# Performance work log

Measured on AMD Instinct MI355X. Metric: run time of the kernel, lower is better.

The kernel has to match this reference:

```python
import jax, jax.numpy as jnp
import numpy as np
import math

HIDDEN = 384
HEADS = 4
HEAD_DIM = HIDDEN // HEADS
B, T = 8, 2048


def _shift_rel(pos_tensor):
    # pos_tensor: [b, h, t, 2t-1] -> [b, h, t, t] (Transformer-XL shift trick)
    b, h, t, n = pos_tensor.shape
    zero_pad = jnp.zeros((b, h, t, 1), dtype=pos_tensor.dtype)
    padded = jnp.concatenate([zero_pad, pos_tensor], axis=-1)  # [b,h,t,n+1]
    padded = padded.reshape(b, h, n + 1, t)
    shifted = padded[:, :, 1:].reshape(b, h, t, n)
    return shifted[:, :, :, : n // 2 + 1]  # [b,h,t,t]


def setup_inputs() -> dict:
    key = jax.random.key(0)
    ks = jax.random.split(key, 12)
    s = 1.0 / math.sqrt(HIDDEN)
    inp = {
        "hidden_states": jax.random.normal(ks[0], (B, T, HIDDEN), jnp.float32),
        "pos_emb": jax.random.normal(ks[1], (1, 2 * T - 1, HIDDEN), jnp.float32),
        "attention_mask": jnp.ones((B, 1, T), jnp.int32),
        "Wq": jax.random.normal(ks[2], (HIDDEN, HIDDEN), jnp.float32) * s,
        "bq": jnp.zeros((HIDDEN,), jnp.float32),
        "Wk": jax.random.normal(ks[3], (HIDDEN, HIDDEN), jnp.float32) * s,
        "bk": jnp.zeros((HIDDEN,), jnp.float32),
        "Wv": jax.random.normal(ks[4], (HIDDEN, HIDDEN), jnp.float32) * s,
        "bv": jnp.zeros((HIDDEN,), jnp.float32),
        "Wo": jax.random.normal(ks[5], (HIDDEN, HIDDEN), jnp.float32) * s,
        "bo": jnp.zeros((HIDDEN,), jnp.float32),
        "Wpos": jax.random.normal(ks[6], (HIDDEN, HIDDEN), jnp.float32) * s,
        "pos_bias_u": jax.random.normal(ks[7], (HEADS, HEAD_DIM), jnp.float32) * s,
        "pos_bias_v": jax.random.normal(ks[8], (HEADS, HEAD_DIM), jnp.float32) * s,
    }
    return inp


def reference(hidden_states, pos_emb, attention_mask, Wq, bq, Wk, bk, Wv, bv,
              Wo, bo, Wpos, pos_bias_u, pos_bias_v):
    bsz, q_len, _ = hidden_states.shape
    # projections (nn.Linear applies x @ W.T + b; weights here stored as [in, out])
    q = (hidden_states @ Wq + bq).reshape(bsz, q_len, HEADS, HEAD_DIM)
    k = (hidden_states @ Wk + bk).reshape(bsz, q_len, HEADS, HEAD_DIM)
    v = (hidden_states @ Wv + bv).reshape(bsz, q_len, HEADS, HEAD_DIM)
    pos = (pos_emb @ Wpos).reshape(pos_emb.shape[0], -1, HEADS, HEAD_DIM)

    q_u = (q + pos_bias_u).transpose(0, 2, 1, 3)  # [b,h,t,d]
    q_v = (q + pos_bias_v).transpose(0, 2, 1, 3)

    # content score: [b,h,t,t]
    matrix_ac = jnp.einsum('bhqd,bkhd->bhqk', q_u, k)
    # position score: [b,h,t,2t-1] then shift
    matrix_bd = jnp.einsum('bhqd,pnhd->bhqn', q_v, pos)
    matrix_bd = _shift_rel(matrix_bd)

    scores = (matrix_ac + matrix_bd) / math.sqrt(HEAD_DIM)

    mask = (attention_mask[:, None] == 0)  # [b,1,1,t]
    min_val = jnp.finfo(scores.dtype).min
    scores = jnp.where(mask, min_val, scores)
    attn = jax.nn.softmax(scores, axis=-1)
    attn = jnp.where(mask, 0.0, attn)

    out = jnp.einsum('bhqk,bkhd->bqhd', attn, v).reshape(bsz, q_len, HIDDEN)
    return out @ Wo + bo
```

## Files before the change

kernel.cpp:

```cpp
#include <hip/hip_runtime.h>
#include <hip/hip_bf16.h>

#define TSEQ 2048
#define HID 384
#define NHEAD 4
#define HD 96
#define NBATCH 8

using bf16 = __bf16;
typedef bf16 bf16x8 __attribute__((ext_vector_type(8)));
typedef bf16 bf16x4 __attribute__((ext_vector_type(4)));
typedef float f32x4 __attribute__((ext_vector_type(4)));
typedef unsigned long long u64;

static __device__ __forceinline__ f32x4 mfma16(bf16x8 a, bf16x8 b, f32x4 c) {
    return __builtin_amdgcn_mfma_f32_16x16x32_bf16(a, b, c, 0, 0, 0);
}

#define LDS_HANDOFF()                                   \
    __builtin_amdgcn_sched_barrier(0x7F);               \
    asm volatile("s_waitcnt lgkmcnt(0)");               \
    __builtin_amdgcn_sched_barrier(0x7F)

#define GL2LDS(g, l) __builtin_amdgcn_global_load_lds(                        \
    (const __attribute__((address_space(1))) unsigned int*)(const void*)(g),  \
    (__attribute__((address_space(3))) unsigned int*)(void*)(l), 16, 0, 0)

__global__ void k_conv8(const float* __restrict__ src, bf16* __restrict__ dst, int n8) {
    int t = blockIdx.x * 256 + threadIdx.x;
    if (t >= n8) return;
    const float4* s4 = reinterpret_cast<const float4*>(src);
    float4 a = s4[2 * t], b = s4[2 * t + 1];
    bf16x8 o;
    o[0] = (bf16)a.x; o[1] = (bf16)a.y; o[2] = (bf16)a.z; o[3] = (bf16)a.w;
    o[4] = (bf16)b.x; o[5] = (bf16)b.y; o[6] = (bf16)b.z; o[7] = (bf16)b.w;
    *reinterpret_cast<bf16x8*>(dst + 8 * t) = o;
}

__global__ void k_convT5(const float* __restrict__ W0, const float* __restrict__ W1,
                         const float* __restrict__ W2, const float* __restrict__ W3,
                         const float* __restrict__ W4,
                         bf16* __restrict__ T0, bf16* __restrict__ T1,
                         bf16* __restrict__ T2, bf16* __restrict__ T3,
                         bf16* __restrict__ T4) {
    int t = blockIdx.x * 256 + threadIdx.x;
    int which = blockIdx.y;
    const float* W = (which == 0) ? W0 : (which == 1) ? W1 : (which == 2) ? W2
                     : (which == 3) ? W3 : W4;
    bf16* T = (which == 0) ? T0 : (which == 1) ? T1 : (which == 2) ? T2
              : (which == 3) ? T3 : T4;
    int n = t / HID, k = t % HID;
    T[t] = (bf16)W[(size_t)k * HID + n];
}

__launch_bounds__(256, 2)
__global__ void k_proj(const bf16* __restrict__ X, const bf16* __restrict__ P,
                       const bf16* __restrict__ wqT, const bf16* __restrict__ wkT,
                       const bf16* __restrict__ wvT, const bf16* __restrict__ wpT,
                       const float* __restrict__ bq, const float* __restrict__ bk,
                       const float* __restrict__ bv,
                       const float* __restrict__ pbu, const float* __restrict__ pbv,
                       bf16* __restrict__ qu, bf16* __restrict__ qv,
                       bf16* __restrict__ kws, bf16* __restrict__ vt,
                       bf16* __restrict__ pp) {
    __shared__ bf16 wt_lds[96][392];
    const float SC = 0.10206207262f;
    int mat = blockIdx.z;
    int m0 = blockIdx.x * 64;
    if (mat == 3 && m0 >= 4095) return;
    int n0 = blockIdx.y * 96;
    const bf16* A  = (mat == 3) ? P : X;
    const bf16* WT = (mat == 0) ? wqT : (mat == 1) ? wkT : (mat == 2) ? wvT : wpT;
    int tid = threadIdx.x;
    #pragma unroll
    for (int s = 0; s < 18; ++s) {
        int cc = tid + 256 * s;
        int r = cc / 48, ch = cc % 48;
        *reinterpret_cast<int4*>(&wt_lds[r][ch * 8]) =
            *reinterpret_cast<const int4*>(WT + (size_t)(n0 + r) * HID + ch * 8);
    }
    __syncthreads();
    int lane = tid & 63, w = tid >> 6;
    int c = lane & 15, g = lane >> 4;
    int arow = m0 + 16 * w + c;
    if (mat == 3 && arow > 4095) arow = 4095;
    const bf16* Abase = A + (size_t)arow * HID + 8 * g;
    f32x4 acc[6] = {};
    for (int ks = 0; ks < 12; ++ks) {
        bf16x8 a = *reinterpret_cast<const bf16x8*>(Abase + 32 * ks);
        #pragma unroll
        for (int jt = 0; jt < 6; ++jt) {
            bf16x8 b = *reinterpret_cast<const bf16x8*>(&wt_lds[16 * jt + c][32 * ks + 8 * g]);
            acc[jt] = mfma16(a, b, acc[jt]);
        }
    }
    int h = blockIdx.y;
    int rbase = m0 + 16 * w + 4 * g;
    if (mat == 0) {
        #pragma unroll
        for (int jt = 0; jt < 6; ++jt) {
            int n = n0 + 16 * jt + c;
            int d = 16 * jt + c;
            float bb = bq[n], bu = pbu[n], bvv = pbv[n];
            #pragma unroll
            for (int j = 0; j < 4; ++j) {
                int m = rbase + j;
                int b_ = m >> 11, t = m & 2047;
                size_t o = (((size_t)(b_ * NHEAD + h)) * TSEQ + t) * HD + d;
                float q = acc[jt][j] + bb;
                qu[o] = (bf16)((q + bu) * SC);
                qv[o] = (bf16)((q + bvv) * SC);
            }
        }
    } else if (mat == 1) {
        #pragma unroll
        for (int jt = 0; jt < 6; ++jt) {
            int n = n0 + 16 * jt + c;
            int d = 16 * jt + c;
            float bb = bk[n];
            #pragma unroll
            for (int j = 0; j < 4; ++j) {
                int m = rbase + j;
                int b_ = m >> 11, t = m & 2047;
                size_t o = (((size_t)(b_ * NHEAD + h)) * TSEQ + t) * HD + d;
                kws[o] = (bf16)(acc[jt][j] + bb);
            }
        }
    } else if (mat == 2) {
        #pragma unroll
        for (int jt = 0; jt < 6; ++jt) {
            int d = 16 * jt + c;
            float bb = bv[n0 + 16 * jt + c];
            int m = rbase;
            int b_ = m >> 11, t0 = m & 2047;
            size_t o = (((size_t)(b_ * NHEAD + h)) * HD + d) * TSEQ + t0;
            bf16x4 pk;
            #pragma unroll
            for (int j = 0; j < 4; ++j) pk[j] = (bf16)(acc[jt][j] + bb);
            *reinterpret_cast<bf16x4*>(vt + o) = pk;
        }
    } else {
        #pragma unroll
        for (int jt = 0; jt < 6; ++jt) {
            int d = 16 * jt + c;
            #pragma unroll
            for (int j = 0; j < 4; ++j) {
                int m = rbase + j;
                if (m < 4095) {
                    size_t o = ((size_t)h * 4096 + m) * HD + d;
                    pp[o] = (bf16)acc[jt][j];
                }
            }
        }
    }
}

__launch_bounds__(256, 2)
__global__ void k_attn(const bf16* __restrict__ qu, const bf16* __restrict__ qv,
                       const bf16* __restrict__ kws, const bf16* __restrict__ vt,
                       const bf16* __restrict__ pp, const int* __restrict__ mask,
                       bf16* __restrict__ out) {
    __shared__ bf16 k_lds[128][104];
    __shared__ bf16 vt_lds[96][128];
    __shared__ bf16 wp_lds[4][16][168];

    int bid = blockIdx.x;
    int x = bid & 7, j5 = bid >> 3;
    int h = x & 3;
    int b_ = (x >> 2) * 4 + (j5 >> 5);
    int qb = j5 & 31;
    int bh = b_ * NHEAD + h;
    int q0 = qb * 64;

    int tid = threadIdx.x, lane = tid & 63, w = tid >> 6;
    int c = lane & 15, g = lane >> 4;
    const float L2E = 1.44269504089f;
    const int NB = 2032 - q0 - 16 * w;

    bf16* k_flat = &k_lds[0][0];
    bf16* vt_flat = &vt_lds[0][0];
    int cc0 = tid, cc1 = tid + 256, cc2 = tid + 512, cc3 = tid + 768;
    int cc4 = tid + 1024, cc5 = tid + 1280, cc6 = tid + 1536;
    int kr0 = cc0 / 13, kc0 = cc0 % 13;  int kO0 = kr0 * HD + (kc0 == 12 ? 0 : kc0 * 8);
    int kr1 = cc1 / 13, kc1 = cc1 % 13;  int kO1 = kr1 * HD + (kc1 == 12 ? 0 : kc1 * 8);
    int kr2 = cc2 / 13, kc2 = cc2 % 13;  int kO2 = kr2 * HD + (kc2 == 12 ? 0 : kc2 * 8);
    int kr3 = cc3 / 13, kc3 = cc3 % 13;  int kO3 = kr3 * HD + (kc3 == 12 ? 0 : kc3 * 8);
    int kr4 = cc4 / 13, kc4 = cc4 % 13;  int kO4 = kr4 * HD + (kc4 == 12 ? 0 : kc4 * 8);
    int kr5 = cc5 / 13, kc5 = cc5 % 13;  int kO5 = kr5 * HD + (kc5 == 12 ? 0 : kc5 * 8);
    int kr6 = cc6 / 13, kc6 = cc6 % 13;  int kO6 = kr6 * HD + (kc6 == 12 ? 0 : kc6 * 8);
    bf16* kL0 = k_flat + (size_t)(64 * w + 0)    * 8;
    bf16* kL1 = k_flat + (size_t)(64 * w + 256)  * 8;
    bf16* kL2 = k_flat + (size_t)(64 * w + 512)  * 8;
    bf16* kL3 = k_flat + (size_t)(64 * w + 768)  * 8;
    bf16* kL4 = k_flat + (size_t)(64 * w + 1024) * 8;
    bf16* kL5 = k_flat + (size_t)(64 * w + 1280) * 8;
    bf16* kL6 = k_flat + (size_t)(64 * w + 1536) * 8;
    bool kAct6 = (w < 2);
    int vr0 = cc0 >> 4, vc0 = cc0 & 15;  int vO0 = vr0 * TSEQ + (vc0 ^ (vr0 & 7)) * 8;
    int vr1 = cc1 >> 4, vc1 = cc1 & 15;  int vO1 = vr1 * TSEQ + (vc1 ^ (vr1 & 7)) * 8;
    int vr2 = cc2 >> 4, vc2 = cc2 & 15;  int vO2 = vr2 * TSEQ + (vc2 ^ (vr2 & 7)) * 8;
    int vr3 = cc3 >> 4, vc3 = cc3 & 15;  int vO3 = vr3 * TSEQ + (vc3 ^ (vr3 & 7)) * 8;
    int vr4 = cc4 >> 4, vc4 = cc4 & 15;  int vO4 = vr4 * TSEQ + (vc4 ^ (vr4 & 7)) * 8;
    int vr5 = cc5 >> 4, vc5 = cc5 & 15;  int vO5 = vr5 * TSEQ + (vc5 ^ (vr5 & 7)) * 8;
    bf16* vL0 = vt_flat + (size_t)(64 * w + 0)    * 8;
    bf16* vL1 = vt_flat + (size_t)(64 * w + 256)  * 8;
    bf16* vL2 = vt_flat + (size_t)(64 * w + 512)  * 8;
    bf16* vL3 = vt_flat + (size_t)(64 * w + 768)  * 8;
    bf16* vL4 = vt_flat + (size_t)(64 * w + 1024) * 8;
    bf16* vL5 = vt_flat + (size_t)(64 * w + 1280) * 8;

    const bf16* kbP = kws + (size_t)bh * TSEQ * HD;
    const bf16* vbP = vt + (size_t)bh * HD * TSEQ;
    const bf16* pbP = pp + (size_t)h * 4096 * HD;
    const int*  mbP = mask + b_ * TSEQ;

    bf16x8 qu_f[3], qv_f[3];
    {
        size_t rowbase = ((size_t)bh * TSEQ + q0 + 16 * w + c) * HD + 8 * g;
        #pragma unroll
        for (int ds = 0; ds < 3; ++ds) {
            qu_f[ds] = *reinterpret_cast<const bf16x8*>(qu + rowbase + 32 * ds);
            qv_f[ds] = *reinterpret_cast<const bf16x8*>(qv + rowbase + 32 * ds);
        }
    }

    f32x4 acc_o[6] = {};
    float mrow = -3.0e38f, lrow = 0.f;
    f32x4 wc;
    int   mk0, mk1;

    bf16* wp_row = &wp_lds[w][c][0];
    const int hc = (15 - c) >> 2;
    const int sh = ((15 - c) & 3) * 16;

    auto winpair = [&](int wb, int ta, int tb) {
        f32x4 wa = {}, wbv = {};
        const bf16* pa = pbP + (size_t)(wb + 16 * ta + c) * HD + 8 * g;
        const bf16* pb = pbP + (size_t)(wb + 16 * tb + c) * HD + 8 * g;
        __builtin_amdgcn_s_setprio(1);
        #pragma unroll
        for (int ds = 0; ds < 3; ++ds) {
            wa  = mfma16(*reinterpret_cast<const bf16x8*>(pa + 32 * ds), qv_f[ds], wa);
            wbv = mfma16(*reinterpret_cast<const bf16x8*>(pb + 32 * ds), qv_f[ds], wbv);
        }
        __builtin_amdgcn_s_setprio(0);
        bf16x4 qa, qb;
        #pragma unroll
        for (int j = 0; j < 4; ++j) { qa[j] = (bf16)wa[j]; qb[j] = (bf16)wbv[j]; }
        *reinterpret_cast<bf16x4*>(wp_row + 16 * ta + 4 * g) = qa;
        *reinterpret_cast<bf16x4*>(wp_row + 16 * tb + 4 * g) = qb;
        return wbv;
    };

    {
        GL2LDS(kbP + kO0, kL0); GL2LDS(kbP + kO1, kL1); GL2LDS(kbP + kO2, kL2);
        GL2LDS(kbP + kO3, kL3); GL2LDS(kbP + kO4, kL4); GL2LDS(kbP + kO5, kL5);
        if (kAct6) GL2LDS(kbP + kO6, kL6);
        GL2LDS(vbP + vO0, vL0); GL2LDS(vbP + vO1, vL1); GL2LDS(vbP + vO2, vL2);
        GL2LDS(vbP + vO3, vL3); GL2LDS(vbP + vO4, vL4); GL2LDS(vbP + vO5, vL5);
        mk0 = mbP[lane]; mk1 = mbP[64 + lane];

        {
            f32x4 w0 = {};
            const bf16* p0 = pbP + (size_t)(NB + c) * HD + 8 * g;
            #pragma unroll
            for (int ds = 0; ds < 3; ++ds)
                w0 = mfma16(*reinterpret_cast<const bf16x8*>(p0 + 32 * ds), qv_f[ds], w0);
            bf16x4 q0v;
            #pragma unroll
            for (int j = 0; j < 4; ++j) q0v[j] = (bf16)w0[j];
            *reinterpret_cast<bf16x4*>(wp_row + 4 * g) = q0v;
        }
        winpair(NB, 1, 2);
        winpair(NB, 3, 4);
        winpair(NB, 5, 6);
        wc = winpair(NB, 7, 8);
    }
    __syncthreads();

    for (int kt = 0; kt < 16; ++kt) {
        unsigned long long bm0 = __ballot(mk0 != 0);
        unsigned long long bm1 = __ballot(mk1 != 0);

        bf16x4 wv[8];
        #pragma unroll
        for (int tk = 0; tk < 8; ++tk) {
            int qd = 4 * tk + g + hc;
            u64 A8 = *reinterpret_cast<const u64*>(wp_row + 4 * qd);
            u64 B8 = *reinterpret_cast<const u64*>(wp_row + 4 * qd + 4);
            u64 o8 = sh ? ((A8 >> sh) | (B8 << (64 - sh))) : A8;
            *reinterpret_cast<u64*>(&wv[tk]) = o8;
        }

        f32x4 acc_s[8];
        #pragma unroll
        for (int tk = 0; tk < 8; ++tk)
            acc_s[tk] = f32x4{(float)wv[tk][0], (float)wv[tk][1],
                              (float)wv[tk][2], (float)wv[tk][3]};
        __builtin_amdgcn_s_setprio(1);
        #pragma unroll
        for (int ds = 0; ds < 3; ++ds) {
            #pragma unroll
            for (int tk = 0; tk < 8; ++tk) {
                bf16x8 a = *reinterpret_cast<const bf16x8*>(
                    &k_lds[16 * tk + c][32 * ds + 8 * g]);
                acc_s[tk] = mfma16(a, qu_f[ds], acc_s[tk]);
            }
        }
        __builtin_amdgcn_s_setprio(0);

        if ((bm0 & bm1) != ~0ull) {
            #pragma unroll
            for (int tk = 0; tk < 8; ++tk) {
                unsigned long long bb = (tk < 4) ? bm0 : bm1;
                int base = 16 * (tk & 3) + 4 * g;
                #pragma unroll
                for (int j = 0; j < 4; ++j)
                    if (!((bb >> (base + j)) & 1)) acc_s[tk][j] = -3.0e38f;
            }
        }
        float pm = acc_s[0][0];
        #pragma unroll
        for (int tk = 0; tk < 8; ++tk)
            #pragma unroll
            for (int j = 0; j < 4; ++j) pm = fmaxf(pm, acc_s[tk][j]);
        pm = fmaxf(pm, __shfl_xor(pm, 16));
        pm = fmaxf(pm, __shfl_xor(pm, 32));
        if (!__all(pm <= mrow + 8.0f)) {
            float mnew = fmaxf(mrow, pm);
            float alpha = exp2f((mrow - mnew) * L2E);
            mrow = mnew; lrow *= alpha;
            #pragma unroll
            for (int ot = 0; ot < 6; ++ot) acc_o[ot] *= alpha;
        }
        float rs = 0.f;
        #pragma unroll
        for (int tk = 0; tk < 8; ++tk)
            #pragma unroll
            for (int j = 0; j < 4; ++j) {
                float p = exp2f((acc_s[tk][j] - mrow) * L2E);
                acc_s[tk][j] = p; rs += p;
            }
        rs += __shfl_xor(rs, 16);
        rs += __shfl_xor(rs, 32);
        lrow += rs;

        #pragma unroll
        for (int tk = 0; tk < 8; ++tk) {
            bf16x4 pk;
            #pragma unroll
            for (int j = 0; j < 4; ++j) pk[j] = (bf16)acc_s[tk][j];
            *reinterpret_cast<bf16x4*>(wp_row + 16 * tk + 4 * g) = pk;
        }
        LDS_HANDOFF();

        __builtin_amdgcn_s_setprio(1);
        #pragma unroll
        for (int ds = 0; ds < 4; ++ds) {
            bf16x8 pb_ = *reinterpret_cast<const bf16x8*>(wp_row + 32 * ds + 8 * g);
            #pragma unroll
            for (int ot = 0; ot < 6; ++ot) {
                int rr = 16 * ot + c;
                bf16x8 a = *reinterpret_cast<const bf16x8*>(
                    &vt_lds[rr][(((4 * ds + g) ^ (rr & 7)) * 8)]);
                acc_o[ot] = mfma16(a, pb_, acc_o[ot]);
            }
        }
        __builtin_amdgcn_s_setprio(0);

        if (kt < 15) {
            __syncthreads();

            int k0n = (kt + 1) * 128;
            const bf16* kb = kbP + (size_t)k0n * HD;
            const bf16* vb = vbP + k0n;
            GL2LDS(kb + kO0, kL0); GL2LDS(kb + kO1, kL1); GL2LDS(kb + kO2, kL2);
            GL2LDS(kb + kO3, kL3); GL2LDS(kb + kO4, kL4); GL2LDS(kb + kO5, kL5);
            if (kAct6) GL2LDS(kb + kO6, kL6);
            GL2LDS(vb + vO0, vL0); GL2LDS(vb + vO1, vL1); GL2LDS(vb + vO2, vL2);
            GL2LDS(vb + vO3, vL3); GL2LDS(vb + vO4, vL4); GL2LDS(vb + vO5, vL5);
            mk0 = mbP[k0n + lane]; mk1 = mbP[k0n + 64 + lane];

            int wb = NB + 128 * (kt + 1);
            bf16x4 q0v;
            #pragma unroll
            for (int j = 0; j < 4; ++j) q0v[j] = (bf16)wc[j];
            *reinterpret_cast<bf16x4*>(wp_row + 4 * g) = q0v;
            winpair(wb, 1, 2);
            winpair(wb, 3, 4);
            winpair(wb, 5, 6);
            wc = winpair(wb, 7, 8);

            __syncthreads();
        }
    }

    float inv = 1.0f / lrow;
    size_t m = (size_t)b_ * TSEQ + q0 + 16 * w + c;
    bf16* ob = out + m * HID + h * HD + 4 * g;
    #pragma unroll
    for (int ot = 0; ot < 6; ++ot) {
        bf16x4 pk;
        #pragma unroll
        for (int j = 0; j < 4; ++j) pk[j] = (bf16)(acc_o[ot][j] * inv);
        *reinterpret_cast<bf16x4*>(&ob[16 * ot]) = pk;
    }
}

__launch_bounds__(256, 2)
__global__ void k_oproj(const bf16* __restrict__ A, const bf16* __restrict__ WT,
                        const float* __restrict__ bias, float* __restrict__ out) {
    __shared__ bf16 wt_lds[96][392];
    int m0 = blockIdx.x * 64, n0 = blockIdx.y * 96;
    int tid = threadIdx.x;
    #pragma unroll
    for (int s = 0; s < 18; ++s) {
        int cc = tid + 256 * s;
        int r = cc / 48, ch = cc % 48;
        *reinterpret_cast<int4*>(&wt_lds[r][ch * 8]) =
            *reinterpret_cast<const int4*>(WT + (size_t)(n0 + r) * HID + ch * 8);
    }
    __syncthreads();
    int lane = tid & 63, w = tid >> 6;
    int c = lane & 15, g = lane >> 4;
    const bf16* Abase = A + (size_t)(m0 + 16 * w + c) * HID + 8 * g;
    f32x4 acc[6] = {};
    for (int ks = 0; ks < 12; ++ks) {
        bf16x8 a = *reinterpret_cast<const bf16x8*>(Abase + 32 * ks);
        #pragma unroll
        for (int jt = 0; jt < 6; ++jt) {
            bf16x8 b = *reinterpret_cast<const bf16x8*>(&wt_lds[16 * jt + c][32 * ks + 8 * g]);
            acc[jt] = mfma16(a, b, acc[jt]);
        }
    }
    int rbase = m0 + 16 * w + 4 * g;
    #pragma unroll
    for (int jt = 0; jt < 6; ++jt) {
        int n = n0 + 16 * jt + c;
        float bb = bias[n];
        #pragma unroll
        for (int j = 0; j < 4; ++j)
            out[(size_t)(rbase + j) * HID + n] = acc[jt][j] + bb;
    }
}

extern "C" void kernel_launch(void* const* d_in, const int* in_sizes, int n_in,
                              void* d_out, int out_size, void* d_ws, size_t ws_size,
                              hipStream_t stream) {
    const float* hs  = (const float*)d_in[0];
    const float* pe  = (const float*)d_in[1];
    const int*   msk = (const int*)d_in[2];
    const float* Wq  = (const float*)d_in[3];
    const float* bq  = (const float*)d_in[4];
    const float* Wk  = (const float*)d_in[5];
    const float* bk  = (const float*)d_in[6];
    const float* Wv  = (const float*)d_in[7];
    const float* bv  = (const float*)d_in[8];
    const float* Wo  = (const float*)d_in[9];
    const float* bo  = (const float*)d_in[10];
    const float* Wp  = (const float*)d_in[11];
    const float* pbu = (const float*)d_in[12];
    const float* pbv = (const float*)d_in[13];

    char* ws = (char*)d_ws;
    size_t off = 0;
    auto alloc = [&](size_t b) { char* p = ws + off; off += (b + 255) & ~(size_t)255; return p; };
    bf16* Xb  = (bf16*)alloc((size_t)16384 * HID * 2);
    bf16* Pb  = (bf16*)alloc((size_t)4096 * HID * 2);
    bf16* wqT = (bf16*)alloc((size_t)HID * HID * 2);
    bf16* wkT = (bf16*)alloc((size_t)HID * HID * 2);
    bf16* wvT = (bf16*)alloc((size_t)HID * HID * 2);
    bf16* woT = (bf16*)alloc((size_t)HID * HID * 2);
    bf16* wpT = (bf16*)alloc((size_t)HID * HID * 2);
    bf16* qu  = (bf16*)alloc((size_t)NBATCH * NHEAD * TSEQ * HD * 2);
    bf16* qv  = (bf16*)alloc((size_t)NBATCH * NHEAD * TSEQ * HD * 2);
    bf16* kws = (bf16*)alloc((size_t)NBATCH * NHEAD * TSEQ * HD * 2);
    bf16* vt  = (bf16*)alloc((size_t)NBATCH * NHEAD * TSEQ * HD * 2);
    bf16* pp  = (bf16*)alloc((size_t)NHEAD * 4096 * HD * 2 + 65536);
    bf16* ao  = (bf16*)alloc((size_t)16384 * HID * 2);

    k_conv8<<<3072, 256, 0, stream>>>(hs, Xb, 786432);
    k_conv8<<<768, 256, 0, stream>>>(pe, Pb, 196560);
    k_convT5<<<dim3(576, 5), 256, 0, stream>>>(Wq, Wk, Wv, Wo, Wp,
                                               wqT, wkT, wvT, woT, wpT);
    k_proj<<<dim3(256, 4, 4), 256, 0, stream>>>(Xb, Pb, wqT, wkT, wvT, wpT,
                                                bq, bk, bv, pbu, pbv,
                                                qu, qv, kws, vt, pp);
    k_attn<<<1024, 256, 0, stream>>>(qu, qv, kws, vt, pp, msk, ao);
    k_oproj<<<dim3(256, 4), 256, 0, stream>>>(ao, woT, bo, (float*)d_out);
}
```

Before: 260.1 us.

## Stage activations in LDS for projections and read K directly from global in attention

The projection kernel now stages a 64-row activation tile in LDS and has each wave handle one head's 96 output columns, with weights read straight from global memory. This quarters the grid and removes redundant activation reloads. The attention kernel drops the K tile from LDS and loads K fragments directly from global/L2 inside the score loop. That frees LDS and removes K staging traffic, but adds uncached-latency global loads on the MFMA critical path and more register pressure from the 4x6 accumulators.

```diff
diff --git a/kernel.cpp b/kernel.cpp
--- a/kernel.cpp
+++ b/kernel.cpp
@@ -63,92 +63,112 @@
                        bf16* __restrict__ qu, bf16* __restrict__ qv,
                        bf16* __restrict__ kws, bf16* __restrict__ vt,
                        bf16* __restrict__ pp) {
-    __shared__ bf16 wt_lds[96][392];
+    __shared__ bf16 a_lds[64][392];
     const float SC = 0.10206207262f;
-    int mat = blockIdx.z;
+    int mat = blockIdx.y;
     int m0 = blockIdx.x * 64;
     if (mat == 3 && m0 >= 4095) return;
-    int n0 = blockIdx.y * 96;
     const bf16* A  = (mat == 3) ? P : X;
     const bf16* WT = (mat == 0) ? wqT : (mat == 1) ? wkT : (mat == 2) ? wvT : wpT;
     int tid = threadIdx.x;
     #pragma unroll
-    for (int s = 0; s < 18; ++s) {
+    for (int s = 0; s < 12; ++s) {
         int cc = tid + 256 * s;
         int r = cc / 48, ch = cc % 48;
-        *reinterpret_cast<int4*>(&wt_lds[r][ch * 8]) =
-            *reinterpret_cast<const int4*>(WT + (size_t)(n0 + r) * HID + ch * 8);
+        int row = m0 + r;
+        if (mat == 3 && row > 4095) row = 4095;
+        *reinterpret_cast<int4*>(&a_lds[r][ch * 8]) =
+            *reinterpret_cast<const int4*>(A + (size_t)row * HID + ch * 8);
     }
     __syncthreads();
     int lane = tid & 63, w = tid >> 6;
     int c = lane & 15, g = lane >> 4;
-    int arow = m0 + 16 * w + c;
-    if (mat == 3 && arow > 4095) arow = 4095;
-    const bf16* Abase = A + (size_t)arow * HID + 8 * g;
-    f32x4 acc[6] = {};
+    int h = w;
+    const bf16* WTb = WT + (size_t)(96 * w) * HID;
+    f32x4 acc[4][6] = {};
     for (int ks = 0; ks < 12; ++ks) {
-        bf16x8 a = *reinterpret_cast<const bf16x8*>(Abase + 32 * ks);
+        bf16x8 b0 = *reinterpret_cast<const bf16x8*>(WTb + (size_t)(c) * HID + 32 * ks + 8 * g);
+        bf16x8 b1 = *reinterpret_cast<const bf16x8*>(WTb + (size_t)(16 + c) * HID + 32 * ks + 8 * g);
+        bf16x8 b2 = *reinterpret_cast<const bf16x8*>(WTb + (size_t)(32 + c) * HID + 32 * ks + 8 * g);
+        bf16x8 b3 = *reinterpret_cast<const bf16x8*>(WTb + (size_t)(48 + c) * HID + 32 * ks + 8 * g);
+        bf16x8 b4 = *reinterpret_cast<const bf16x8*>(WTb + (size_t)(64 + c) * HID + 32 * ks + 8 * g);
+        bf16x8 b5 = *reinterpret_cast<const bf16x8*>(WTb + (size_t)(80 + c) * HID + 32 * ks + 8 * g);
+        #pragma unroll
+        for (int i = 0; i < 4; ++i) {
+            bf16x8 a = *reinterpret_cast<const bf16x8*>(&a_lds[16 * i + c][32 * ks + 8 * g]);
+            acc[i][0] = mfma16(a, b0, acc[i][0]);
+            acc[i][1] = mfma16(a, b1, acc[i][1]);
+            acc[i][2] = mfma16(a, b2, acc[i][2]);
+            acc[i][3] = mfma16(a, b3, acc[i][3]);
+            acc[i][4] = mfma16(a, b4, acc[i][4]);
+            acc[i][5] = mfma16(a, b5, acc[i][5]);
+        }
+    }
+    if (mat == 0) {
         #pragma unroll
         for (int jt = 0; jt < 6; ++jt) {
-            bf16x8 b = *reinterpret_cast<const bf16x8*>(&wt_lds[16 * jt + c][32 * ks + 8 * g]);
-            acc[jt] = mfma16(a, b, acc[jt]);
-        }
-    }
-    int h = blockIdx.y;
-    int rbase = m0 + 16 * w + 4 * g;
-    if (mat == 0) {
-        #pragma unroll
-        for (int jt = 0; jt < 6; ++jt) {
-            int n = n0 + 16 * jt + c;
+            int n = 96 * h + 16 * jt + c;
             int d = 16 * jt + c;
             float bb = bq[n], bu = pbu[n], bvv = pbv[n];
             #pragma unroll
-            for (int j = 0; j < 4; ++j) {
-                int m = rbase + j;
-                int b_ = m >> 11, t = m & 2047;
-                size_t o = (((size_t)(b_ * NHEAD + h)) * TSEQ + t) * HD + d;
-                float q = acc[jt][j] + bb;
-                qu[o] = (bf16)((q + bu) * SC);
-                qv[o] = (bf16)((q + bvv) * SC);
+            for (int i = 0; i < 4; ++i) {
+                #pragma unroll
+                for (int j = 0; j < 4; ++j) {
+                    int m = m0 + 16 * i + 4 * g + j;
+                    int b_ = m >> 11, t = m & 2047;
+                    size_t o = (((size_t)(b_ * NHEAD + h)) * TSEQ + t) * HD + d;
+                    float q = acc[i][jt][j] + bb;
+                    qu[o] = (bf16)((q + bu) * SC);
+                    qv[o] = (bf16)((q + bvv) * SC);
+                }
             }
         }
     } else if (mat == 1) {
         #pragma unroll
         for (int jt = 0; jt < 6; ++jt) {
-            int n = n0 + 16 * jt + c;
+            int n = 96 * h + 16 * jt + c;
             int d = 16 * jt + c;
             float bb = bk[n];
             #pragma unroll
-            for (int j = 0; j < 4; ++j) {
-                int m = rbase + j;
-                int b_ = m >> 11, t = m & 2047;
-                size_t o = (((size_t)(b_ * NHEAD + h)) * TSEQ + t) * HD + d;
-                kws[o] = (bf16)(acc[jt][j] + bb);
+            for (int i = 0; i < 4; ++i) {
+                #pragma unroll
+                for (int j = 0; j < 4; ++j) {
+                    int m = m0 + 16 * i + 4 * g + j;
+                    int b_ = m >> 11, t = m & 2047;
+                    size_t o = (((size_t)(b_ * NHEAD + h)) * TSEQ + t) * HD + d;
+                    kws[o] = (bf16)(acc[i][jt][j] + bb);
+                }
             }
         }
     } else if (mat == 2) {
         #pragma unroll
         for (int jt = 0; jt < 6; ++jt) {
             int d = 16 * jt + c;
-            float bb = bv[n0 + 16 * jt + c];
-            int m = rbase;
-            int b_ = m >> 11, t0 = m & 2047;
-            size_t o = (((size_t)(b_ * NHEAD + h)) * HD + d) * TSEQ + t0;
-            bf16x4 pk;
-            #pragma unroll
-            for (int j = 0; j < 4; ++j) pk[j] = (bf16)(acc[jt][j] + bb);
-            *reinterpret_cast<bf16x4*>(vt + o) = pk;
+            float bb = bv[96 * h + 16 * jt + c];
+            #pragma unroll
+            for (int i = 0; i < 4; ++i) {
+                int m = m0 + 16 * i + 4 * g;
+                int b_ = m >> 11, t0 = m & 2047;
+                size_t o = (((size_t)(b_ * NHEAD + h)) * HD + d) * TSEQ + t0;
+                bf16x4 pk;
+                #pragma unroll
+                for (int j = 0; j < 4; ++j) pk[j] = (bf16)(acc[i][jt][j] + bb);
+                *reinterpret_cast<bf16x4*>(vt + o) = pk;
+            }
         }
     } else {
         #pragma unroll
         for (int jt = 0; jt < 6; ++jt) {
             int d = 16 * jt + c;
             #pragma unroll
-            for (int j = 0; j < 4; ++j) {
-                int m = rbase + j;
-                if (m < 4095) {
-                    size_t o = ((size_t)h * 4096 + m) * HD + d;
-                    pp[o] = (bf16)acc[jt][j];
+            for (int i = 0; i < 4; ++i) {
+                #pragma unroll
+                for (int j = 0; j < 4; ++j) {
+                    int m = m0 + 16 * i + 4 * g + j;
+                    if (m < 4095) {
+                        size_t o = ((size_t)h * 4096 + m) * HD + d;
+                        pp[o] = (bf16)acc[i][jt][j];
+                    }
                 }
             }
         }
@@ -160,7 +180,6 @@
                        const bf16* __restrict__ kws, const bf16* __restrict__ vt,
                        const bf16* __restrict__ pp, const int* __restrict__ mask,
                        bf16* __restrict__ out) {
-    __shared__ bf16 k_lds[128][104];
     __shared__ bf16 vt_lds[96][128];
     __shared__ bf16 wp_lds[4][16][168];
 
@@ -177,25 +196,9 @@
     const float L2E = 1.44269504089f;
     const int NB = 2032 - q0 - 16 * w;
 
-    bf16* k_flat = &k_lds[0][0];
     bf16* vt_flat = &vt_lds[0][0];
-    int cc0 = tid, cc1 = tid + 256, cc2 = tid + 512, cc3 = tid + 768;
-    int cc4 = tid + 1024, cc5 = tid + 1280, cc6 = tid + 1536;
-    int kr0 = cc0 / 13, kc0 = cc0 % 13;  int kO0 = kr0 * HD + (kc0 == 12 ? 0 : kc0 * 8);
-    int kr1 = cc1 / 13, kc1 = cc1 % 13;  int kO1 = kr1 * HD + (kc1 == 12 ? 0 : kc1 * 8);
-    int kr2 = cc2 / 13, kc2 = cc2 % 13;  int kO2 = kr2 * HD + (kc2 == 12 ? 0 : kc2 * 8);
-    int kr3 = cc3 / 13, kc3 = cc3 % 13;  int kO3 = kr3 * HD + (kc3 == 12 ? 0 : kc3 * 8);
-    int kr4 = cc4 / 13, kc4 = cc4 % 13;  int kO4 = kr4 * HD + (kc4 == 12 ? 0 : kc4 * 8);
-    int kr5 = cc5 / 13, kc5 = cc5 % 13;  int kO5 = kr5 * HD + (kc5 == 12 ? 0 : kc5 * 8);
-    int kr6 = cc6 / 13, kc6 = cc6 % 13;  int kO6 = kr6 * HD + (kc6 == 12 ? 0 : kc6 * 8);
-    bf16* kL0 = k_flat + (size_t)(64 * w + 0)    * 8;
-    bf16* kL1 = k_flat + (size_t)(64 * w + 256)  * 8;
-    bf16* kL2 = k_flat + (size_t)(64 * w + 512)  * 8;
-    bf16* kL3 = k_flat + (size_t)(64 * w + 768)  * 8;
-    bf16* kL4 = k_flat + (size_t)(64 * w + 1024) * 8;
-    bf16* kL5 = k_flat + (size_t)(64 * w + 1280) * 8;
-    bf16* kL6 = k_flat + (size_t)(64 * w + 1536) * 8;
-    bool kAct6 = (w < 2);
+    int cc0 = tid, cc1 = tid + 256, cc2 = tid + 512;
+    int cc3 = tid + 768, cc4 = tid + 1024, cc5 = tid + 1280;
     int vr0 = cc0 >> 4, vc0 = cc0 & 15;  int vO0 = vr0 * TSEQ + (vc0 ^ (vr0 & 7)) * 8;
     int vr1 = cc1 >> 4, vc1 = cc1 & 15;  int vO1 = vr1 * TSEQ + (vc1 ^ (vr1 & 7)) * 8;
     int vr2 = cc2 >> 4, vc2 = cc2 & 15;  int vO2 = vr2 * TSEQ + (vc2 ^ (vr2 & 7)) * 8;
@@ -253,9 +256,6 @@
     };
 
     {
-        GL2LDS(kbP + kO0, kL0); GL2LDS(kbP + kO1, kL1); GL2LDS(kbP + kO2, kL2);
-        GL2LDS(kbP + kO3, kL3); GL2LDS(kbP + kO4, kL4); GL2LDS(kbP + kO5, kL5);
-        if (kAct6) GL2LDS(kbP + kO6, kL6);
         GL2LDS(vbP + vO0, vL0); GL2LDS(vbP + vO1, vL1); GL2LDS(vbP + vO2, vL2);
         GL2LDS(vbP + vO3, vL3); GL2LDS(vbP + vO4, vL4); GL2LDS(vbP + vO5, vL5);
         mk0 = mbP[lane]; mk1 = mbP[64 + lane];
@@ -279,6 +279,7 @@
     __syncthreads();
 
     for (int kt = 0; kt < 16; ++kt) {
+        int k0 = kt * 128;
         unsigned long long bm0 = __ballot(mk0 != 0);
         unsigned long long bm1 = __ballot(mk1 != 0);
 
@@ -303,7 +304,7 @@
             #pragma unroll
             for (int tk = 0; tk < 8; ++tk) {
                 bf16x8 a = *reinterpret_cast<const bf16x8*>(
-                    &k_lds[16 * tk + c][32 * ds + 8 * g]);
+                    kbP + (size_t)(k0 + 16 * tk + c) * HD + 32 * ds + 8 * g);
                 acc_s[tk] = mfma16(a, qu_f[ds], acc_s[tk]);
             }
         }
@@ -371,12 +372,8 @@
         if (kt < 15) {
             __syncthreads();
 
-            int k0n = (kt + 1) * 128;
-            const bf16* kb = kbP + (size_t)k0n * HD;
+            int k0n = k0 + 128;
             const bf16* vb = vbP + k0n;
-            GL2LDS(kb + kO0, kL0); GL2LDS(kb + kO1, kL1); GL2LDS(kb + kO2, kL2);
-            GL2LDS(kb + kO3, kL3); GL2LDS(kb + kO4, kL4); GL2LDS(kb + kO5, kL5);
-            if (kAct6) GL2LDS(kb + kO6, kL6);
             GL2LDS(vb + vO0, vL0); GL2LDS(vb + vO1, vL1); GL2LDS(vb + vO2, vL2);
             GL2LDS(vb + vO3, vL3); GL2LDS(vb + vO4, vL4); GL2LDS(vb + vO5, vL5);
             mk0 = mbP[k0n + lane]; mk1 = mbP[k0n + 64 + lane];
@@ -483,9 +480,9 @@
     k_conv8<<<768, 256, 0, stream>>>(pe, Pb, 196560);
     k_convT5<<<dim3(576, 5), 256, 0, stream>>>(Wq, Wk, Wv, Wo, Wp,
                                                wqT, wkT, wvT, woT, wpT);
-    k_proj<<<dim3(256, 4, 4), 256, 0, stream>>>(Xb, Pb, wqT, wkT, wvT, wpT,
-                                                bq, bk, bv, pbu, pbv,
-                                                qu, qv, kws, vt, pp);
+    k_proj<<<dim3(256, 4), 256, 0, stream>>>(Xb, Pb, wqT, wkT, wvT, wpT,
+                                             bq, bk, bv, pbu, pbv,
+                                             qu, qv, kws, vt, pp);
     k_attn<<<1024, 256, 0, stream>>>(qu, qv, kws, vt, pp, msk, ao);
     k_oproj<<<dim3(256, 4), 256, 0, stream>>>(ao, woT, bo, (float*)d_out);
 }
```

After: 344.2 us. 32.4% more time.
